# Kernel tuning notes

Hardware: AMD Instinct MI355X
Metric: run time of the kernel (lower is better)

## Reference

```python
import jax, jax.numpy as jnp
import numpy as np

BATCH, PART, OUT_NODES, IN_NODES = 256, 128, 64, 64

def setup_inputs() -> dict:
    key = jax.random.key(0)
    k1, k2 = jax.random.split(key)
    x = jax.random.normal(k1, (BATCH, PART, IN_NODES), dtype=jnp.float32)
    weight = 0.1 * jax.random.normal(k2, (PART, OUT_NODES, IN_NODES), dtype=jnp.float32)
    return {"x": x, "weight": weight}

def reference(x, weight):
    # w: log-softmax over input-node axis -> [regions, out_nodes, in_nodes]
    w = jax.nn.log_softmax(weight, axis=2)
    # broadcast add: [batch, regions, 1, in_nodes] + [regions, out_nodes, in_nodes]
    # then logsumexp over in_nodes -> [batch, regions, out_nodes]
    return jax.scipy.special.logsumexp(x[:, :, None, :] + w[None], axis=-1)
```

## Files before the change

kernel.cpp:

```cpp
#include <hip/hip_runtime.h>
#include <hip/hip_bf16.h>

#define NPART 128
#define NBATCH 256
#define NOUT 64
#define NIN 64
#define LDK 72

typedef __attribute__((ext_vector_type(8))) short short8;
typedef __attribute__((ext_vector_type(4))) float floatx4;
typedef __attribute__((ext_vector_type(8))) unsigned short ushort8;

__device__ __forceinline__ unsigned short f_to_bf16(float f) {
    union { unsigned int i; float f; } v; v.f = f;
    unsigned int b = v.i;
    unsigned int r = b + 0x7FFFu + ((b >> 16) & 1u);
    return (unsigned short)(r >> 16);
}

__global__ __launch_bounds__(256, 2) void sumlayer_kernel(
    const float* __restrict__ x,
    const float* __restrict__ w,
    float* __restrict__ out)
{
    __shared__ alignas(16) unsigned short Alds[64 * LDK];
    __shared__ alignas(16) unsigned short Wlds[64 * LDK];
    __shared__ float wlse[64];

    const int p  = blockIdx.x;
    const int b0 = blockIdx.y * 64;
    const int t  = threadIdx.x;
    const int row = t >> 2;
    const int sub = t & 3;

    {
        const float* wrow = w + (((size_t)p * NOUT + row) * NIN + sub * 16);
        float vals[16];
        #pragma unroll
        for (int j = 0; j < 16; j += 4) {
            float4 v = *(const float4*)(wrow + j);
            vals[j] = v.x; vals[j+1] = v.y; vals[j+2] = v.z; vals[j+3] = v.w;
        }
        float s = 0.f;
        ushort8 e0, e1;
        #pragma unroll
        for (int j = 0; j < 8; ++j) {
            float e = __expf(vals[j]);     s += e; e0[j] = f_to_bf16(e);
        }
        #pragma unroll
        for (int j = 0; j < 8; ++j) {
            float e = __expf(vals[8 + j]); s += e; e1[j] = f_to_bf16(e);
        }
        unsigned short* dst = Wlds + row * LDK + sub * 16;
        *(ushort8*)(dst)     = e0;
        *(ushort8*)(dst + 8) = e1;
        s += __shfl_xor(s, 1);
        s += __shfl_xor(s, 2);
        if (sub == 0) wlse[row] = __logf(s);
    }

    {
        const float* xrow = x + ((((size_t)(b0 + row)) * NPART + p) * NIN + sub * 16);
        float vals[16];
        #pragma unroll
        for (int j = 0; j < 16; j += 4) {
            float4 v = *(const float4*)(xrow + j);
            vals[j] = v.x; vals[j+1] = v.y; vals[j+2] = v.z; vals[j+3] = v.w;
        }
        ushort8 a0, a1;
        #pragma unroll
        for (int j = 0; j < 8; ++j) a0[j] = f_to_bf16(__expf(vals[j]));
        #pragma unroll
        for (int j = 0; j < 8; ++j) a1[j] = f_to_bf16(__expf(vals[8 + j]));
        unsigned short* dst = Alds + row * LDK + sub * 16;
        *(ushort8*)(dst)     = a0;
        *(ushort8*)(dst + 8) = a1;
    }

    __syncthreads();

    const int wv = t >> 6;
    const int l  = t & 63;
    const int ln = l & 15;
    const int q  = l >> 4;
    const int m0 = wv * 16;

    const short8 a0 = *(const short8*)(Alds + (m0 + ln) * LDK + q * 8);
    const short8 a1 = *(const short8*)(Alds + (m0 + ln) * LDK + 32 + q * 8);

    floatx4 acc[4];
    #pragma unroll
    for (int ot = 0; ot < 4; ++ot) {
        const short8 bb0 = *(const short8*)(Wlds + (ot * 16 + ln) * LDK + q * 8);
        const short8 bb1 = *(const short8*)(Wlds + (ot * 16 + ln) * LDK + 32 + q * 8);
        floatx4 c = {0.f, 0.f, 0.f, 0.f};
        c = __builtin_amdgcn_mfma_f32_16x16x32_bf16(a0, bb0, c, 0, 0, 0);
        c = __builtin_amdgcn_mfma_f32_16x16x32_bf16(a1, bb1, c, 0, 0, 0);
        acc[ot] = c;
    }

    #pragma unroll
    for (int ot = 0; ot < 4; ++ot) {
        const int o = ot * 16 + ln;
        const float wl = wlse[o];
        #pragma unroll
        for (int r = 0; r < 4; ++r) {
            const int b = b0 + m0 + q * 4 + r;
            out[(((size_t)b) * NPART + p) * NOUT + o] = __logf(acc[ot][r]) - wl;
        }
    }
}

extern "C" void kernel_launch(void* const* d_in, const int* in_sizes, int n_in,
                              void* d_out, int out_size, void* d_ws, size_t ws_size,
                              hipStream_t stream) {
    const float* x = (const float*)d_in[0];
    const float* w = (const float*)d_in[1];
    float* out = (float*)d_out;
    dim3 grid(NPART, NBATCH / 64);
    sumlayer_kernel<<<grid, dim3(256), 0, stream>>>(x, w, out);
}
```

Baseline: 64.11 us.

## Load MFMA fragments straight from global memory, drop LDS staging, halve batch tile

Each wave now loads its x and weight rows from global memory directly in MFMA operand layout, applies exp and the bf16 conversion in registers, and computes the weight log-sum with cross-lane shuffles. This removes the shared-memory staging, the LDS reads and the block barrier. The batch tile per block drops from 64 to 32 and waves split into 2x2 row/output tiles, doubling the grid, with launch bounds raised to 4 blocks. In exchange, weight rows are loaded and exponentiated by more waves and blocks (redundant global reads and exp work), and the stores become smaller scattered writes.

Measured after the change: 66.42 us. +3.6%, slower.

```diff
diff --git a/kernel.cpp b/kernel.cpp
--- a/kernel.cpp
+++ b/kernel.cpp
@@ -1,112 +1,85 @@
 #include <hip/hip_runtime.h>
-#include <hip/hip_bf16.h>
 
 #define NPART 128
 #define NBATCH 256
 #define NOUT 64
 #define NIN 64
-#define LDK 72
 
 typedef __attribute__((ext_vector_type(8))) short short8;
 typedef __attribute__((ext_vector_type(4))) float floatx4;
-typedef __attribute__((ext_vector_type(8))) unsigned short ushort8;
 
-__device__ __forceinline__ unsigned short f_to_bf16(float f) {
+__device__ __forceinline__ short f_to_bf16(float f) {
     union { unsigned int i; float f; } v; v.f = f;
     unsigned int b = v.i;
     unsigned int r = b + 0x7FFFu + ((b >> 16) & 1u);
-    return (unsigned short)(r >> 16);
+    return (short)(r >> 16);
 }
 
-__global__ __launch_bounds__(256, 2) void sumlayer_kernel(
+__global__ __launch_bounds__(256, 4) void sumlayer_kernel(
     const float* __restrict__ x,
     const float* __restrict__ w,
     float* __restrict__ out)
 {
-    __shared__ alignas(16) unsigned short Alds[64 * LDK];
-    __shared__ alignas(16) unsigned short Wlds[64 * LDK];
-    __shared__ float wlse[64];
-
     const int p  = blockIdx.x;
-    const int b0 = blockIdx.y * 64;
+    const int b0 = blockIdx.y * 32;
     const int t  = threadIdx.x;
-    const int row = t >> 2;
-    const int sub = t & 3;
-
-    {
-        const float* wrow = w + (((size_t)p * NOUT + row) * NIN + sub * 16);
-        float vals[16];
-        #pragma unroll
-        for (int j = 0; j < 16; j += 4) {
-            float4 v = *(const float4*)(wrow + j);
-            vals[j] = v.x; vals[j+1] = v.y; vals[j+2] = v.z; vals[j+3] = v.w;
-        }
-        float s = 0.f;
-        ushort8 e0, e1;
-        #pragma unroll
-        for (int j = 0; j < 8; ++j) {
-            float e = __expf(vals[j]);     s += e; e0[j] = f_to_bf16(e);
-        }
-        #pragma unroll
-        for (int j = 0; j < 8; ++j) {
-            float e = __expf(vals[8 + j]); s += e; e1[j] = f_to_bf16(e);
-        }
-        unsigned short* dst = Wlds + row * LDK + sub * 16;
-        *(ushort8*)(dst)     = e0;
-        *(ushort8*)(dst + 8) = e1;
-        s += __shfl_xor(s, 1);
-        s += __shfl_xor(s, 2);
-        if (sub == 0) wlse[row] = __logf(s);
-    }
-
-    {
-        const float* xrow = x + ((((size_t)(b0 + row)) * NPART + p) * NIN + sub * 16);
-        float vals[16];
-        #pragma unroll
-        for (int j = 0; j < 16; j += 4) {
-            float4 v = *(const float4*)(xrow + j);
-            vals[j] = v.x; vals[j+1] = v.y; vals[j+2] = v.z; vals[j+3] = v.w;
-        }
-        ushort8 a0, a1;
-        #pragma unroll
-        for (int j = 0; j < 8; ++j) a0[j] = f_to_bf16(__expf(vals[j]));
-        #pragma unroll
-        for (int j = 0; j < 8; ++j) a1[j] = f_to_bf16(__expf(vals[8 + j]));
-        unsigned short* dst = Alds + row * LDK + sub * 16;
-        *(ushort8*)(dst)     = a0;
-        *(ushort8*)(dst + 8) = a1;
-    }
-
-    __syncthreads();
-
     const int wv = t >> 6;
     const int l  = t & 63;
     const int ln = l & 15;
     const int q  = l >> 4;
-    const int m0 = wv * 16;
+    const int r0 = (wv & 1) * 16;
+    const int oh = (wv >> 1) * 32;
 
-    const short8 a0 = *(const short8*)(Alds + (m0 + ln) * LDK + q * 8);
-    const short8 a1 = *(const short8*)(Alds + (m0 + ln) * LDK + 32 + q * 8);
+    const float* xrow = x + (((size_t)(b0 + r0 + ln) * NPART + p) * NIN);
+    float4 xa0 = *(const float4*)(xrow + q * 8);
+    float4 xa1 = *(const float4*)(xrow + q * 8 + 4);
+    float4 xa2 = *(const float4*)(xrow + 32 + q * 8);
+    float4 xa3 = *(const float4*)(xrow + 32 + q * 8 + 4);
+    short8 af0, af1;
+    {
+        const float v0[8] = {xa0.x, xa0.y, xa0.z, xa0.w, xa1.x, xa1.y, xa1.z, xa1.w};
+        const float v1[8] = {xa2.x, xa2.y, xa2.z, xa2.w, xa3.x, xa3.y, xa3.z, xa3.w};
+        #pragma unroll
+        for (int j = 0; j < 8; ++j) af0[j] = f_to_bf16(__expf(v0[j]));
+        #pragma unroll
+        for (int j = 0; j < 8; ++j) af1[j] = f_to_bf16(__expf(v1[j]));
+    }
 
-    floatx4 acc[4];
+    floatx4 acc[2];
+    float wl[2];
     #pragma unroll
-    for (int ot = 0; ot < 4; ++ot) {
-        const short8 bb0 = *(const short8*)(Wlds + (ot * 16 + ln) * LDK + q * 8);
-        const short8 bb1 = *(const short8*)(Wlds + (ot * 16 + ln) * LDK + 32 + q * 8);
+    for (int ot = 0; ot < 2; ++ot) {
+        const int o = oh + ot * 16 + ln;
+        const float* wrow = w + (((size_t)p * NOUT + o) * NIN);
+        float4 wb0 = *(const float4*)(wrow + q * 8);
+        float4 wb1 = *(const float4*)(wrow + q * 8 + 4);
+        float4 wb2 = *(const float4*)(wrow + 32 + q * 8);
+        float4 wb3 = *(const float4*)(wrow + 32 + q * 8 + 4);
+        const float v0[8] = {wb0.x, wb0.y, wb0.z, wb0.w, wb1.x, wb1.y, wb1.z, wb1.w};
+        const float v1[8] = {wb2.x, wb2.y, wb2.z, wb2.w, wb3.x, wb3.y, wb3.z, wb3.w};
+        short8 bf0, bf1;
+        float s = 0.f;
+        #pragma unroll
+        for (int j = 0; j < 8; ++j) { float e = __expf(v0[j]); s += e; bf0[j] = f_to_bf16(e); }
+        #pragma unroll
+        for (int j = 0; j < 8; ++j) { float e = __expf(v1[j]); s += e; bf1[j] = f_to_bf16(e); }
+        s += __shfl_xor(s, 16);
+        s += __shfl_xor(s, 32);
+        wl[ot] = __logf(s);
+
         floatx4 c = {0.f, 0.f, 0.f, 0.f};
-        c = __builtin_amdgcn_mfma_f32_16x16x32_bf16(a0, bb0, c, 0, 0, 0);
-        c = __builtin_amdgcn_mfma_f32_16x16x32_bf16(a1, bb1, c, 0, 0, 0);
+        c = __builtin_amdgcn_mfma_f32_16x16x32_bf16(af0, bf0, c, 0, 0, 0);
+        c = __builtin_amdgcn_mfma_f32_16x16x32_bf16(af1, bf1, c, 0, 0, 0);
         acc[ot] = c;
     }
 
     #pragma unroll
-    for (int ot = 0; ot < 4; ++ot) {
-        const int o = ot * 16 + ln;
-        const float wl = wlse[o];
+    for (int ot = 0; ot < 2; ++ot) {
+        const int o = oh + ot * 16 + ln;
         #pragma unroll
         for (int r = 0; r < 4; ++r) {
-            const int b = b0 + m0 + q * 4 + r;
-            out[(((size_t)b) * NPART + p) * NOUT + o] = __logf(acc[ot][r]) - wl;
+            const int b = b0 + r0 + q * 4 + r;
+            out[((size_t)b * NPART + p) * NOUT + o] = __logf(acc[ot][r]) - wl[ot];
         }
     }
 }
@@ -117,6 +90,6 @@
     const float* x = (const float*)d_in[0];
     const float* w = (const float*)d_in[1];
     float* out = (float*)d_out;
-    dim3 grid(NPART, NBATCH / 64);
+    dim3 grid(NPART, NBATCH / 32);
     sumlayer_kernel<<<grid, dim3(256), 0, stream>>>(x, w, out);
 }
```
